# Optimization experiments

Hardware: AMD Instinct MI355X
Metric: run time of the kernel (lower is better)

Reference implementation:

```python
import jax, jax.numpy as jnp
import numpy as np

B, L, H, NH, NB = 16, 200, 128, 2, 2
ITEMS, SPAN = 50000, 256
NEG = -2.0**32 + 1.0  # mask value used by the torch module


def _ln(x, g, b, eps=1e-8):
    m = jnp.mean(x, axis=-1, keepdims=True)
    v = jnp.mean((x - m) ** 2, axis=-1, keepdims=True)
    return (x - m) / jnp.sqrt(v + eps) * g + b


def setup_inputs() -> dict:
    key = jax.random.key(0)
    ks = jax.random.split(key, 20)
    p = lambda k, s: (jax.random.normal(k, s, jnp.float32) * 0.02)
    item_emb = p(ks[0], (ITEMS + 1, H)).at[0].set(0.0)  # padding_idx=0
    return {
        "user_ids": jax.random.randint(ks[1], (B,), 0, 10000),
        "log_seqs": jax.random.randint(ks[2], (B, L), 0, ITEMS),
        "time_matrices": jax.random.randint(ks[3], (B, L, L), 0, SPAN),
        "pos_seqs": jax.random.randint(ks[4], (B, L), 0, ITEMS),
        "neg_seqs": jax.random.randint(ks[5], (B, L), 0, ITEMS),
        "item_emb": item_emb,
        "pos_K_emb": p(ks[6], (L, H)),
        "pos_V_emb": p(ks[7], (L, H)),
        "time_K_emb": p(ks[8], (SPAN + 1, H)),
        "time_V_emb": p(ks[9], (SPAN + 1, H)),
        "Wq": p(ks[10], (NB, H, H)), "bq": jnp.zeros((NB, H)),
        "Wk": p(ks[11], (NB, H, H)), "bk": jnp.zeros((NB, H)),
        "Wv": p(ks[12], (NB, H, H)), "bv": jnp.zeros((NB, H)),
        "ln1_g": jnp.ones((NB, H)), "ln1_b": jnp.zeros((NB, H)),
        "W1": p(ks[13], (NB, H, H)), "b1": jnp.zeros((NB, H)),
        "W2": p(ks[14], (NB, H, H)), "b2": jnp.zeros((NB, H)),
        "ln2_g": jnp.ones((NB, H)), "ln2_b": jnp.zeros((NB, H)),
        "lnf_g": jnp.ones((H,)), "lnf_b": jnp.zeros((H,)),
    }


def reference(user_ids, log_seqs, time_matrices, pos_seqs, neg_seqs,
              item_emb, pos_K_emb, pos_V_emb, time_K_emb, time_V_emb,
              Wq, bq, Wk, bk, Wv, bv, ln1_g, ln1_b,
              W1, b1, W2, b2, ln2_g, ln2_b, lnf_g, lnf_b):
    d = H // NH
    pad = (log_seqs == 0)                    # (B,L) timeline mask
    keep = (~pad)[..., None].astype(jnp.float32)

    seqs = item_emb[log_seqs] * jnp.sqrt(jnp.float32(H))
    seqs = seqs * keep
    posK = pos_K_emb.reshape(L, NH, d)       # same for every batch element
    posV = pos_V_emb.reshape(L, NH, d)
    tmK = time_K_emb[time_matrices].reshape(B, L, L, NH, d)  # (B,L,L,h,d)
    tmV = time_V_emb[time_matrices].reshape(B, L, L, NH, d)
    causal = ~jnp.tril(jnp.ones((L, L), dtype=bool))          # True = masked
    mask = pad[:, None, :, None] | causal[None, None, :, :]   # (B,1,L,L) row-mask | causal

    for i in range(NB):
        Q = (seqs @ Wq[i].T + bq[i]).reshape(B, L, NH, d)
        K = (seqs @ Wk[i].T + bk[i]).reshape(B, L, NH, d)
        V = (seqs @ Wv[i].T + bv[i]).reshape(B, L, NH, d)
        aw = jnp.einsum('bqhd,bkhd->bhqk', Q, K)
        aw = aw + jnp.einsum('bqhd,khd->bhqk', Q, posK)
        aw = aw + jnp.einsum('bqkhd,bqhd->bhqk', tmK, Q)
        aw = aw / jnp.sqrt(jnp.float32(d))
        aw = jnp.where(mask, NEG, aw)
        A = jax.nn.softmax(aw, axis=-1)                        # (B,h,L,L)
        out = jnp.einsum('bhqk,bkhd->bqhd', A, V)
        out = out + jnp.einsum('bhqk,khd->bqhd', A, posV)
        out = out + jnp.einsum('bhqk,bqkhd->bqhd', A, tmV)
        out = out.reshape(B, L, H)
        seqs = _ln(seqs + out, ln1_g[i], ln1_b[i])
        ffn = jax.nn.relu(seqs @ W1[i].T + b1[i]) @ W2[i].T + b2[i]
        seqs = _ln(seqs + ffn, ln2_g[i], ln2_b[i])
        seqs = seqs * keep

    log_feats = _ln(seqs, lnf_g, lnf_b)
    pos_logits = jnp.sum(log_feats * item_emb[pos_seqs], axis=-1)  # (B,L)
    neg_logits = jnp.sum(log_feats * item_emb[neg_seqs], axis=-1)
    return jnp.stack([pos_logits, neg_logits])  # (2,B,L)
```

## Files before the change

### kernel.cpp

```cpp
#include <hip/hip_runtime.h>
#include <hip/hip_bf16.h>
#include <math.h>

#define BB 16
#define LL 200
#define HH 128
#define DD 64
#define QT2 8
#define NQT2 25
#define NEGF -4294967295.0f
#define SQRTH 11.313708498984761f

__global__ __launch_bounds__(512) void k_qkv(float* __restrict__ seqs,
    const int* __restrict__ log_seqs, const float* __restrict__ item_emb, int do_embed,
    const float* __restrict__ Wq, const float* __restrict__ bq,
    const float* __restrict__ Wk, const float* __restrict__ bk,
    const float* __restrict__ Wv, const float* __restrict__ bv,
    const float* __restrict__ posK, const float* __restrict__ posV,
    float* __restrict__ Q, float* __restrict__ Kp, float* __restrict__ Vp) {
    __shared__ float s_lds[16][HH];
    int r0g = blockIdx.x * 16;
    int t = threadIdx.x;
    if (do_embed) {
        int r = t >> 5, d4 = t & 31;
        int id = log_seqs[r0g + r];
        float4 v = make_float4(0.f, 0.f, 0.f, 0.f);
        if (id != 0) {
            v = ((const float4*)(item_emb + id * HH))[d4];
            v.x *= SQRTH; v.y *= SQRTH; v.z *= SQRTH; v.w *= SQRTH;
        }
        *(float4*)&s_lds[r][d4 * 4] = v;
        ((float4*)(seqs + r0g * HH))[t] = v;
    } else {
        ((float4*)s_lds)[t] = ((const float4*)(seqs + r0g * HH))[t];
    }
    __syncthreads();
    int c = t & 127, rg = t >> 7;
    float aq[4] = {0.f, 0.f, 0.f, 0.f};
    float ak[4] = {0.f, 0.f, 0.f, 0.f};
    float av[4] = {0.f, 0.f, 0.f, 0.f};
    const float4* wq4 = (const float4*)(Wq + c * HH);
    const float4* wk4 = (const float4*)(Wk + c * HH);
    const float4* wv4 = (const float4*)(Wv + c * HH);
#pragma unroll 4
    for (int k4 = 0; k4 < HH / 4; ++k4) {
        float4 wq = wq4[k4], wk = wk4[k4], wv = wv4[k4];
#pragma unroll
        for (int r = 0; r < 4; ++r) {
            float4 s = *(const float4*)&s_lds[rg * 4 + r][k4 * 4];
            aq[r] += s.x * wq.x + s.y * wq.y + s.z * wq.z + s.w * wq.w;
            ak[r] += s.x * wk.x + s.y * wk.y + s.z * wk.z + s.w * wk.w;
            av[r] += s.x * wv.x + s.y * wv.y + s.z * wv.z + s.w * wv.w;
        }
    }
#pragma unroll
    for (int r = 0; r < 4; ++r) {
        int row = r0g + rg * 4 + r;
        int l = row % LL;
        Q[row * HH + c]  = aq[r] + bq[c];
        Kp[row * HH + c] = ak[r] + bk[c] + posK[l * HH + c];
        Vp[row * HH + c] = av[r] + bv[c] + posV[l * HH + c];
    }
}

__global__ __launch_bounds__(256) void k_proj(const float* __restrict__ Q,
    const float* __restrict__ timeK, float* __restrict__ projK) {
    int bh = blockIdx.x / 13, qt = blockIdx.x % 13;
    int b = bh >> 1, h = bh & 1;
    int qlo = qt * 16;
    __shared__ float Qs[16][68];
    __shared__ float TK[32][68];
    int t = threadIdx.x;
    {
        int r = t >> 4, d4 = t & 15;
        int q = qlo + r;
        float4 v = make_float4(0.f, 0.f, 0.f, 0.f);
        if (q < LL) v = ((const float4*)(Q + (b * LL + q) * HH + h * DD))[d4];
        *(float4*)&Qs[r][d4 * 4] = v;
    }
    int tq = t >> 4, ttl = t & 15;
    int q = qlo + tq;
    for (int c = 0; c < 9; ++c) {
        int base = c * 32;
        __syncthreads();
        for (int x = t; x < 512; x += 256) {
            int i = x >> 4, d4 = x & 15;
            int tt = base + i;
            if (tt < 257)
                *(float4*)&TK[i][d4 * 4] =
                    ((const float4*)(timeK + tt * HH + h * DD))[d4];
        }
        __syncthreads();
#pragma unroll
        for (int j = 0; j < 2; ++j) {
            int ti = ttl + 16 * j;
            int tt = base + ti;
            if (tt < 257 && q < LL) {
                float acc = 0.f;
#pragma unroll
                for (int d4 = 0; d4 < 16; ++d4) {
                    float4 qv = *(const float4*)&Qs[tq][d4 * 4];
                    float4 kv = *(const float4*)&TK[ti][d4 * 4];
                    acc += qv.x * kv.x + qv.y * kv.y + qv.z * kv.z + qv.w * kv.w;
                }
                projK[(bh * LL + q) * 257 + tt] = acc;
            }
        }
    }
}

__global__ __launch_bounds__(256) void k_attn(
    const float* __restrict__ Q, const float* __restrict__ Kp, const float* __restrict__ Vp,
    const float* __restrict__ projK, const float* __restrict__ timeV,
    const int* __restrict__ tm, const int* __restrict__ log_seqs,
    float* __restrict__ attnout) {
    int bh = blockIdx.x / NQT2, qt = blockIdx.x % NQT2;
    int b = bh >> 1, h = bh & 1;
    int qlo = qt * QT2;
    __shared__ float K_s[32][68];
    __shared__ float smemW[457 * 12];
    __shared__ unsigned long long pm64[4];
    __shared__ int s_allmask;
#define WT(i, j) smemW[(i) * 12 + (j)]
    int t = threadIdx.x;
    int tq = t >> 5, lane = t & 31, g = tq;
    int q = qlo + tq;
    int qhi = qlo + QT2 - 1;

    {
        bool keep = (t < LL) && (log_seqs[b * LL + t] != 0);
        unsigned long long ball = __ballot(keep);
        if ((t & 63) == 0) pm64[t >> 6] = ball;
    }
    if (t == 0) s_allmask = 0;
    for (int x = t; x < 200 * 12; x += 256) smemW[x] = NEGF;
    for (int x = 200 * 12 + t; x < 457 * 12; x += 256) smemW[x] = 0.f;
    float4 qreg[16];
    {
        const float4* qp = (const float4*)(Q + (b * LL + q) * HH + h * DD);
#pragma unroll
        for (int d4 = 0; d4 < 16; ++d4) qreg[d4] = qp[d4];
    }
    const int* tmrow = tm + (b * LL + q) * LL;
    const float* projrow = projK + (bh * LL + q) * 257;
    __syncthreads();

    int nkc = (qhi >> 5) + 1;
    for (int kc = 0; kc < nkc; ++kc) {
        int kbase = kc * 32;
        for (int x = t; x < 512; x += 256) {
            int i = x >> 4, d4 = x & 15;
            int k = kbase + i;
            if (k < LL)
                *(float4*)&K_s[i][d4 * 4] =
                    ((const float4*)(Kp + (b * LL + k) * HH + h * DD))[d4];
        }
        __syncthreads();
        int k = kbase + lane;
        if (k <= q && ((pm64[k >> 6] >> (k & 63)) & 1ull)) {
            float acc = 0.f;
#pragma unroll
            for (int d4 = 0; d4 < 16; ++d4) {
                float4 kv = *(const float4*)&K_s[lane][d4 * 4];
                acc += qreg[d4].x * kv.x + qreg[d4].y * kv.y +
                       qreg[d4].z * kv.z + qreg[d4].w * kv.w;
            }
            WT(k, tq) = (acc + projrow[tmrow[k]]) * 0.125f;
        }
        __syncthreads();
    }

    float mx = -INFINITY;
    for (int k = lane; k < LL; k += 32) mx = fmaxf(mx, WT(k, tq));
    mx = fmaxf(mx, __shfl_xor(mx, 1, 64));
    mx = fmaxf(mx, __shfl_xor(mx, 2, 64));
    mx = fmaxf(mx, __shfl_xor(mx, 4, 64));
    mx = fmaxf(mx, __shfl_xor(mx, 8, 64));
    mx = fmaxf(mx, __shfl_xor(mx, 16, 64));
    bool allmask = (mx == NEGF);
    float sum = 0.f;
    for (int k = lane; k < LL; k += 32) {
        float e = __expf(WT(k, tq) - mx);
        WT(k, tq) = e;
        sum += e;
    }
    sum += __shfl_xor(sum, 1, 64);
    sum += __shfl_xor(sum, 2, 64);
    sum += __shfl_xor(sum, 4, 64);
    sum += __shfl_xor(sum, 8, 64);
    sum += __shfl_xor(sum, 16, 64);
    float inv = 1.0f / sum;
    int klim = allmask ? LL : (q + 1);
    if (allmask && lane == 0) s_allmask = 1;
    for (int k = lane; k < LL; k += 32) {
        float p = WT(k, tq) * inv;
        WT(k, tq) = p;
        if (k < klim) atomicAdd(&WT(200 + tmrow[k], tq), p);
    }
    __syncthreads();

    int kmax = s_allmask ? LL : (qhi + 1);
    float a00=0.f,a01=0.f,a10=0.f,a11=0.f,a20=0.f,a21=0.f,a30=0.f,a31=0.f;
    float a40=0.f,a41=0.f,a50=0.f,a51=0.f,a60=0.f,a61=0.f,a70=0.f,a71=0.f;
#define PV_STEP(WROW, SRCPTR)                                            \
    {                                                                    \
        const float* wr = &WROW;                                         \
        float4 w0 = *(const float4*)wr;                                  \
        float4 w1 = *(const float4*)(wr + 4);                            \
        float2 vv = *(const float2*)(SRCPTR);                            \
        a00 += w0.x * vv.x; a01 += w0.x * vv.y;                          \
        a10 += w0.y * vv.x; a11 += w0.y * vv.y;                          \
        a20 += w0.z * vv.x; a21 += w0.z * vv.y;                          \
        a30 += w0.w * vv.x; a31 += w0.w * vv.y;                          \
        a40 += w1.x * vv.x; a41 += w1.x * vv.y;                          \
        a50 += w1.y * vv.x; a51 += w1.y * vv.y;                          \
        a60 += w1.z * vv.x; a61 += w1.z * vv.y;                          \
        a70 += w1.w * vv.x; a71 += w1.w * vv.y;                          \
    }
    for (int i = g; i < kmax; i += 8)
        PV_STEP(WT(i, 0), Vp + (b * LL + i) * HH + h * DD + lane * 2);
    for (int i = g; i < 257; i += 8)
        PV_STEP(WT(200 + i, 0), timeV + i * HH + h * DD + lane * 2);
#undef PV_STEP
    __syncthreads();
    float* part = smemW;
    part[g * 512 + 0 * 64 + lane * 2] = a00; part[g * 512 + 0 * 64 + lane * 2 + 1] = a01;
    part[g * 512 + 1 * 64 + lane * 2] = a10; part[g * 512 + 1 * 64 + lane * 2 + 1] = a11;
    part[g * 512 + 2 * 64 + lane * 2] = a20; part[g * 512 + 2 * 64 + lane * 2 + 1] = a21;
    part[g * 512 + 3 * 64 + lane * 2] = a30; part[g * 512 + 3 * 64 + lane * 2 + 1] = a31;
    part[g * 512 + 4 * 64 + lane * 2] = a40; part[g * 512 + 4 * 64 + lane * 2 + 1] = a41;
    part[g * 512 + 5 * 64 + lane * 2] = a50; part[g * 512 + 5 * 64 + lane * 2 + 1] = a51;
    part[g * 512 + 6 * 64 + lane * 2] = a60; part[g * 512 + 6 * 64 + lane * 2 + 1] = a61;
    part[g * 512 + 7 * 64 + lane * 2] = a70; part[g * 512 + 7 * 64 + lane * 2 + 1] = a71;
    __syncthreads();
    {
        float ox = 0.f, oy = 0.f;
#pragma unroll
        for (int gg = 0; gg < 8; ++gg) {
            ox += part[gg * 512 + tq * 64 + lane * 2];
            oy += part[gg * 512 + tq * 64 + lane * 2 + 1];
        }
        *(float2*)(attnout + (b * LL + q) * HH + h * DD + lane * 2) =
            make_float2(ox, oy);
    }
#undef WT
}

__global__ __launch_bounds__(512) void k_ffn_full(
    float* __restrict__ seqs, const float* __restrict__ AO,
    const float* __restrict__ g1, const float* __restrict__ be1,
    const float* __restrict__ W1, const float* __restrict__ b1,
    const float* __restrict__ W2, const float* __restrict__ b2,
    const float* __restrict__ g2, const float* __restrict__ be2,
    const int* __restrict__ log_seqs, int do_final,
    const float* __restrict__ lnf_g, const float* __restrict__ lnf_b,
    const float* __restrict__ item_emb,
    const int* __restrict__ pos_seqs, const int* __restrict__ neg_seqs,
    float* __restrict__ out) {
    __shared__ float s_lds[16][HH];
    __shared__ float h_lds[16][HH];
    int r0g = blockIdx.x * 16;
    int t = threadIdx.x;
    {
        float4 a = ((const float4*)(seqs + r0g * HH))[t];
        float4 o = ((const float4*)(AO + r0g * HH))[t];
        a.x += o.x; a.y += o.y; a.z += o.z; a.w += o.w;
        ((float4*)s_lds)[t] = a;
    }
    __syncthreads();
    int w = t >> 6, lane = t & 63;
    int lrow = w * 2 + (lane >> 5), cl = lane & 31;
    {
        float sm = 0.f;
#pragma unroll
        for (int j = 0; j < 4; ++j) sm += s_lds[lrow][cl + 32 * j];
        sm += __shfl_xor(sm, 1, 64);
        sm += __shfl_xor(sm, 2, 64);
        sm += __shfl_xor(sm, 4, 64);
        sm += __shfl_xor(sm, 8, 64);
        sm += __shfl_xor(sm, 16, 64);
        float mean = sm * (1.0f / HH);
        float vr = 0.f;
#pragma unroll
        for (int j = 0; j < 4; ++j) {
            float d = s_lds[lrow][cl + 32 * j] - mean;
            vr += d * d;
        }
        vr += __shfl_xor(vr, 1, 64);
        vr += __shfl_xor(vr, 2, 64);
        vr += __shfl_xor(vr, 4, 64);
        vr += __shfl_xor(vr, 8, 64);
        vr += __shfl_xor(vr, 16, 64);
        float rstd = rsqrtf(vr * (1.0f / HH) + 1e-8f);
#pragma unroll
        for (int j = 0; j < 4; ++j) {
            int c = cl + 32 * j;
            s_lds[lrow][c] = (s_lds[lrow][c] - mean) * rstd * g1[c] + be1[c];
        }
    }
    __syncthreads();
    int c = t & 127, rg = t >> 7;
    float acc[4] = {0.f, 0.f, 0.f, 0.f};
    const float4* w14 = (const float4*)(W1 + c * HH);
#pragma unroll 4
    for (int k4 = 0; k4 < HH / 4; ++k4) {
        float4 ww = w14[k4];
#pragma unroll
        for (int r = 0; r < 4; ++r) {
            float4 s = *(const float4*)&s_lds[rg * 4 + r][k4 * 4];
            acc[r] += s.x * ww.x + s.y * ww.y + s.z * ww.z + s.w * ww.w;
        }
    }
#pragma unroll
    for (int r = 0; r < 4; ++r) h_lds[rg * 4 + r][c] = fmaxf(acc[r] + b1[c], 0.f);
    __syncthreads();
#pragma unroll
    for (int r = 0; r < 4; ++r) acc[r] = 0.f;
    const float4* w24 = (const float4*)(W2 + c * HH);
#pragma unroll 4
    for (int k4 = 0; k4 < HH / 4; ++k4) {
        float4 ww = w24[k4];
#pragma unroll
        for (int r = 0; r < 4; ++r) {
            float4 s = *(const float4*)&h_lds[rg * 4 + r][k4 * 4];
            acc[r] += s.x * ww.x + s.y * ww.y + s.z * ww.z + s.w * ww.w;
        }
    }
    __syncthreads();
#pragma unroll
    for (int r = 0; r < 4; ++r)
        h_lds[rg * 4 + r][c] = s_lds[rg * 4 + r][c] + acc[r] + b2[c];
    __syncthreads();
    {
        float sm = 0.f;
#pragma unroll
        for (int j = 0; j < 4; ++j) sm += h_lds[lrow][cl + 32 * j];
        sm += __shfl_xor(sm, 1, 64);
        sm += __shfl_xor(sm, 2, 64);
        sm += __shfl_xor(sm, 4, 64);
        sm += __shfl_xor(sm, 8, 64);
        sm += __shfl_xor(sm, 16, 64);
        float mean = sm * (1.0f / HH);
        float vr = 0.f;
#pragma unroll
        for (int j = 0; j < 4; ++j) {
            float d = h_lds[lrow][cl + 32 * j] - mean;
            vr += d * d;
        }
        vr += __shfl_xor(vr, 1, 64);
        vr += __shfl_xor(vr, 2, 64);
        vr += __shfl_xor(vr, 4, 64);
        vr += __shfl_xor(vr, 8, 64);
        vr += __shfl_xor(vr, 16, 64);
        float rstd = rsqrtf(vr * (1.0f / HH) + 1e-8f);
        int row = r0g + lrow;
        float keep = (log_seqs[row] != 0) ? 1.0f : 0.0f;
        float y2[4];
#pragma unroll
        for (int j = 0; j < 4; ++j) {
            int cc = cl + 32 * j;
            y2[j] = ((h_lds[lrow][cc] - mean) * rstd * g2[cc] + be2[cc]) * keep;
        }
        if (!do_final) {
#pragma unroll
            for (int j = 0; j < 4; ++j)
                seqs[row * HH + cl + 32 * j] = y2[j];
        } else {
            float sm2 = y2[0] + y2[1] + y2[2] + y2[3];
            sm2 += __shfl_xor(sm2, 1, 64);
            sm2 += __shfl_xor(sm2, 2, 64);
            sm2 += __shfl_xor(sm2, 4, 64);
            sm2 += __shfl_xor(sm2, 8, 64);
            sm2 += __shfl_xor(sm2, 16, 64);
            float mean2 = sm2 * (1.0f / HH);
            float vr2 = 0.f;
#pragma unroll
            for (int j = 0; j < 4; ++j) {
                float d = y2[j] - mean2;
                vr2 += d * d;
            }
            vr2 += __shfl_xor(vr2, 1, 64);
            vr2 += __shfl_xor(vr2, 2, 64);
            vr2 += __shfl_xor(vr2, 4, 64);
            vr2 += __shfl_xor(vr2, 8, 64);
            vr2 += __shfl_xor(vr2, 16, 64);
            float rstd2 = rsqrtf(vr2 * (1.0f / HH) + 1e-8f);
            int pid = pos_seqs[row];
            int nid = neg_seqs[row];
            float pp = 0.f, nn = 0.f;
#pragma unroll
            for (int j = 0; j < 4; ++j) {
                int cc = cl + 32 * j;
                float lf = (y2[j] - mean2) * rstd2 * lnf_g[cc] + lnf_b[cc];
                pp += lf * item_emb[pid * HH + cc];
                nn += lf * item_emb[nid * HH + cc];
            }
            pp += __shfl_xor(pp, 1, 64);
            pp += __shfl_xor(pp, 2, 64);
            pp += __shfl_xor(pp, 4, 64);
            pp += __shfl_xor(pp, 8, 64);
            pp += __shfl_xor(pp, 16, 64);
            nn += __shfl_xor(nn, 1, 64);
            nn += __shfl_xor(nn, 2, 64);
            nn += __shfl_xor(nn, 4, 64);
            nn += __shfl_xor(nn, 8, 64);
            nn += __shfl_xor(nn, 16, 64);
            if (cl == 0) {
                out[row] = pp;
                out[BB * LL + row] = nn;
            }
        }
    }
}

extern "C" void kernel_launch(void* const* d_in, const int* in_sizes, int n_in,
                              void* d_out, int out_size, void* d_ws, size_t ws_size,
                              hipStream_t stream) {
    const int* log_seqs = (const int*)d_in[1];
    const int* tm       = (const int*)d_in[2];
    const int* pos_seqs = (const int*)d_in[3];
    const int* neg_seqs = (const int*)d_in[4];
    const float* item_emb = (const float*)d_in[5];
    const float* posK   = (const float*)d_in[6];
    const float* posV   = (const float*)d_in[7];
    const float* timeK  = (const float*)d_in[8];
    const float* timeV  = (const float*)d_in[9];
    const float* Wq = (const float*)d_in[10];
    const float* bq = (const float*)d_in[11];
    const float* Wk = (const float*)d_in[12];
    const float* bk = (const float*)d_in[13];
    const float* Wv = (const float*)d_in[14];
    const float* bv = (const float*)d_in[15];
    const float* ln1_g = (const float*)d_in[16];
    const float* ln1_b = (const float*)d_in[17];
    const float* W1 = (const float*)d_in[18];
    const float* b1 = (const float*)d_in[19];
    const float* W2 = (const float*)d_in[20];
    const float* b2 = (const float*)d_in[21];
    const float* ln2_g = (const float*)d_in[22];
    const float* ln2_b = (const float*)d_in[23];
    const float* lnf_g = (const float*)d_in[24];
    const float* lnf_b = (const float*)d_in[25];

    float* ws    = (float*)d_ws;
    float* seqs  = ws;
    float* Qb    = seqs + 409600;
    float* Kpb   = Qb + 409600;
    float* Vpb   = Kpb + 409600;
    float* AO    = Vpb + 409600;
    float* projK = AO + 409600;

    for (int i = 0; i < 2; ++i) {
        k_qkv<<<BB * LL / 16, 512, 0, stream>>>(seqs, log_seqs, item_emb,
            (i == 0) ? 1 : 0,
            Wq + i * HH * HH, bq + i * HH,
            Wk + i * HH * HH, bk + i * HH,
            Wv + i * HH * HH, bv + i * HH,
            posK, posV, Qb, Kpb, Vpb);
        k_proj<<<32 * 13, 256, 0, stream>>>(Qb, timeK, projK);
        k_attn<<<32 * NQT2, 256, 0, stream>>>(Qb, Kpb, Vpb, projK, timeV,
                                              tm, log_seqs, AO);
        k_ffn_full<<<BB * LL / 16, 512, 0, stream>>>(seqs, AO,
            ln1_g + i * HH, ln1_b + i * HH,
            W1 + i * HH * HH, b1 + i * HH,
            W2 + i * HH * HH, b2 + i * HH,
            ln2_g + i * HH, ln2_b + i * HH, log_seqs,
            (i == 1) ? 1 : 0, lnf_g, lnf_b, item_emb,
            pos_seqs, neg_seqs, (float*)d_out);
    }
}
```

Baseline: 197.8 us.

## Shrink per-block row tiles across all kernels to raise grid parallelism

All four kernels now take smaller row or query tiles. QKV and FFN blocks handle 4 rows instead of 16, the projection handles 8 queries instead of 16, and attention handles 4 queries with 128 threads instead of 8 with 256. QKV now gives each of three 128-thread groups one of the Q, K or V weight matrices. Attention reads the padding mask from global memory instead of building a ballot bitmask, and reuses the K tile buffer for the partial-sum reduction. The goal is many more blocks to fill the GPU's compute units, at the cost of reading each weight matrix from memory more times per block and less reuse of shared tiles.

```diff
diff --git a/kernel.cpp b/kernel.cpp
--- a/kernel.cpp
+++ b/kernel.cpp
@@ -6,82 +6,83 @@
 #define LL 200
 #define HH 128
 #define DD 64
-#define QT2 8
-#define NQT2 25
+#define NQT4 50
 #define NEGF -4294967295.0f
 #define SQRTH 11.313708498984761f
 
-__global__ __launch_bounds__(512) void k_qkv(float* __restrict__ seqs,
+__global__ __launch_bounds__(384) void k_qkv(float* __restrict__ seqs,
     const int* __restrict__ log_seqs, const float* __restrict__ item_emb, int do_embed,
     const float* __restrict__ Wq, const float* __restrict__ bq,
     const float* __restrict__ Wk, const float* __restrict__ bk,
     const float* __restrict__ Wv, const float* __restrict__ bv,
     const float* __restrict__ posK, const float* __restrict__ posV,
     float* __restrict__ Q, float* __restrict__ Kp, float* __restrict__ Vp) {
-    __shared__ float s_lds[16][HH];
-    int r0g = blockIdx.x * 16;
+    __shared__ float s_lds[4][HH];
+    int r0g = blockIdx.x * 4;
     int t = threadIdx.x;
-    if (do_embed) {
+    if (t < 128) {
         int r = t >> 5, d4 = t & 31;
-        int id = log_seqs[r0g + r];
-        float4 v = make_float4(0.f, 0.f, 0.f, 0.f);
-        if (id != 0) {
-            v = ((const float4*)(item_emb + id * HH))[d4];
-            v.x *= SQRTH; v.y *= SQRTH; v.z *= SQRTH; v.w *= SQRTH;
-        }
-        *(float4*)&s_lds[r][d4 * 4] = v;
-        ((float4*)(seqs + r0g * HH))[t] = v;
-    } else {
-        ((float4*)s_lds)[t] = ((const float4*)(seqs + r0g * HH))[t];
-    }
-    __syncthreads();
-    int c = t & 127, rg = t >> 7;
-    float aq[4] = {0.f, 0.f, 0.f, 0.f};
-    float ak[4] = {0.f, 0.f, 0.f, 0.f};
-    float av[4] = {0.f, 0.f, 0.f, 0.f};
-    const float4* wq4 = (const float4*)(Wq + c * HH);
-    const float4* wk4 = (const float4*)(Wk + c * HH);
-    const float4* wv4 = (const float4*)(Wv + c * HH);
-#pragma unroll 4
-    for (int k4 = 0; k4 < HH / 4; ++k4) {
-        float4 wq = wq4[k4], wk = wk4[k4], wv = wv4[k4];
-#pragma unroll
-        for (int r = 0; r < 4; ++r) {
-            float4 s = *(const float4*)&s_lds[rg * 4 + r][k4 * 4];
-            aq[r] += s.x * wq.x + s.y * wq.y + s.z * wq.z + s.w * wq.w;
-            ak[r] += s.x * wk.x + s.y * wk.y + s.z * wk.z + s.w * wk.w;
-            av[r] += s.x * wv.x + s.y * wv.y + s.z * wv.z + s.w * wv.w;
-        }
-    }
+        if (do_embed) {
+            int id = log_seqs[r0g + r];
+            float4 v = make_float4(0.f, 0.f, 0.f, 0.f);
+            if (id != 0) {
+                v = ((const float4*)(item_emb + id * HH))[d4];
+                v.x *= SQRTH; v.y *= SQRTH; v.z *= SQRTH; v.w *= SQRTH;
+            }
+            *(float4*)&s_lds[r][d4 * 4] = v;
+            ((float4*)(seqs + r0g * HH))[t] = v;
+        } else {
+            ((float4*)s_lds)[t] = ((const float4*)(seqs + r0g * HH))[t];
+        }
+    }
+    __syncthreads();
+    int which = t >> 7, col = t & 127;
+    const float* W = (which == 0) ? Wq : (which == 1) ? Wk : Wv;
+    float a0 = 0.f, a1 = 0.f, a2 = 0.f, a3 = 0.f;
+    const float4* w4 = (const float4*)(W + col * HH);
+#pragma unroll 8
+    for (int k4 = 0; k4 < 32; ++k4) {
+        float4 w = w4[k4];
+        float4 s0 = *(const float4*)&s_lds[0][k4 * 4];
+        float4 s1 = *(const float4*)&s_lds[1][k4 * 4];
+        float4 s2 = *(const float4*)&s_lds[2][k4 * 4];
+        float4 s3 = *(const float4*)&s_lds[3][k4 * 4];
+        a0 += s0.x * w.x + s0.y * w.y + s0.z * w.z + s0.w * w.w;
+        a1 += s1.x * w.x + s1.y * w.y + s1.z * w.z + s1.w * w.w;
+        a2 += s2.x * w.x + s2.y * w.y + s2.z * w.z + s2.w * w.w;
+        a3 += s3.x * w.x + s3.y * w.y + s3.z * w.z + s3.w * w.w;
+    }
+    float a[4] = {a0, a1, a2, a3};
 #pragma unroll
     for (int r = 0; r < 4; ++r) {
-        int row = r0g + rg * 4 + r;
+        int row = r0g + r;
         int l = row % LL;
-        Q[row * HH + c]  = aq[r] + bq[c];
-        Kp[row * HH + c] = ak[r] + bk[c] + posK[l * HH + c];
-        Vp[row * HH + c] = av[r] + bv[c] + posV[l * HH + c];
+        if (which == 0) {
+            Q[row * HH + col] = a[r] + bq[col];
+        } else if (which == 1) {
+            Kp[row * HH + col] = a[r] + bk[col] + posK[l * HH + col];
+        } else {
+            Vp[row * HH + col] = a[r] + bv[col] + posV[l * HH + col];
+        }
     }
 }
 
 __global__ __launch_bounds__(256) void k_proj(const float* __restrict__ Q,
     const float* __restrict__ timeK, float* __restrict__ projK) {
-    int bh = blockIdx.x / 13, qt = blockIdx.x % 13;
+    int bh = blockIdx.x / 25, qt = blockIdx.x % 25;
     int b = bh >> 1, h = bh & 1;
-    int qlo = qt * 16;
-    __shared__ float Qs[16][68];
+    int qlo = qt * 8;
+    __shared__ float Qs[8][68];
     __shared__ float TK[32][68];
     int t = threadIdx.x;
-    {
+    if (t < 128) {
         int r = t >> 4, d4 = t & 15;
-        int q = qlo + r;
-        float4 v = make_float4(0.f, 0.f, 0.f, 0.f);
-        if (q < LL) v = ((const float4*)(Q + (b * LL + q) * HH + h * DD))[d4];
-        *(float4*)&Qs[r][d4 * 4] = v;
-    }
-    int tq = t >> 4, ttl = t & 15;
-    int q = qlo + tq;
-    for (int c = 0; c < 9; ++c) {
-        int base = c * 32;
+        *(float4*)&Qs[r][d4 * 4] =
+            ((const float4*)(Q + (b * LL + qlo + r) * HH + h * DD))[d4];
+    }
+    int tq = t >> 5, ttl = t & 31;
+    for (int ch = 0; ch < 9; ++ch) {
+        int base = ch * 32;
         __syncthreads();
         for (int x = t; x < 512; x += 256) {
             int i = x >> 4, d4 = x & 15;
@@ -91,50 +92,40 @@
                     ((const float4*)(timeK + tt * HH + h * DD))[d4];
         }
         __syncthreads();
+        int tt = base + ttl;
+        if (tt < 257) {
+            float acc = 0.f;
 #pragma unroll
-        for (int j = 0; j < 2; ++j) {
-            int ti = ttl + 16 * j;
-            int tt = base + ti;
-            if (tt < 257 && q < LL) {
-                float acc = 0.f;
-#pragma unroll
-                for (int d4 = 0; d4 < 16; ++d4) {
-                    float4 qv = *(const float4*)&Qs[tq][d4 * 4];
-                    float4 kv = *(const float4*)&TK[ti][d4 * 4];
-                    acc += qv.x * kv.x + qv.y * kv.y + qv.z * kv.z + qv.w * kv.w;
-                }
-                projK[(bh * LL + q) * 257 + tt] = acc;
+            for (int d4 = 0; d4 < 16; ++d4) {
+                float4 qv = *(const float4*)&Qs[tq][d4 * 4];
+                float4 kv = *(const float4*)&TK[ttl][d4 * 4];
+                acc += qv.x * kv.x + qv.y * kv.y + qv.z * kv.z + qv.w * kv.w;
             }
+            projK[(bh * LL + qlo + tq) * 257 + tt] = acc;
         }
     }
 }
 
-__global__ __launch_bounds__(256) void k_attn(
+__global__ __launch_bounds__(128) void k_attn(
     const float* __restrict__ Q, const float* __restrict__ Kp, const float* __restrict__ Vp,
     const float* __restrict__ projK, const float* __restrict__ timeV,
     const int* __restrict__ tm, const int* __restrict__ log_seqs,
     float* __restrict__ attnout) {
-    int bh = blockIdx.x / NQT2, qt = blockIdx.x % NQT2;
+    int bh = blockIdx.x / NQT4, qt = blockIdx.x % NQT4;
     int b = bh >> 1, h = bh & 1;
-    int qlo = qt * QT2;
+    int qlo = qt * 4;
     __shared__ float K_s[32][68];
-    __shared__ float smemW[457 * 12];
-    __shared__ unsigned long long pm64[4];
+    __shared__ float smemW[457 * 8];
     __shared__ int s_allmask;
-#define WT(i, j) smemW[(i) * 12 + (j)]
+#define WT(i, j) smemW[(i) * 8 + (j)]
     int t = threadIdx.x;
     int tq = t >> 5, lane = t & 31, g = tq;
     int q = qlo + tq;
-    int qhi = qlo + QT2 - 1;
-
-    {
-        bool keep = (t < LL) && (log_seqs[b * LL + t] != 0);
-        unsigned long long ball = __ballot(keep);
-        if ((t & 63) == 0) pm64[t >> 6] = ball;
-    }
+    int qhi = qlo + 3;
+
     if (t == 0) s_allmask = 0;
-    for (int x = t; x < 200 * 12; x += 256) smemW[x] = NEGF;
-    for (int x = 200 * 12 + t; x < 457 * 12; x += 256) smemW[x] = 0.f;
+    for (int x = t; x < 200 * 8; x += 128) smemW[x] = NEGF;
+    for (int x = 200 * 8 + t; x < 457 * 8; x += 128) smemW[x] = 0.f;
     float4 qreg[16];
     {
         const float4* qp = (const float4*)(Q + (b * LL + q) * HH + h * DD);
@@ -143,12 +134,13 @@
     }
     const int* tmrow = tm + (b * LL + q) * LL;
     const float* projrow = projK + (bh * LL + q) * 257;
+    const int* lsrow = log_seqs + b * LL;
     __syncthreads();
 
     int nkc = (qhi >> 5) + 1;
     for (int kc = 0; kc < nkc; ++kc) {
         int kbase = kc * 32;
-        for (int x = t; x < 512; x += 256) {
+        for (int x = t; x < 512; x += 128) {
             int i = x >> 4, d4 = x & 15;
             int k = kbase + i;
             if (k < LL)
@@ -157,7 +149,7 @@
         }
         __syncthreads();
         int k = kbase + lane;
-        if (k <= q && ((pm64[k >> 6] >> (k & 63)) & 1ull)) {
+        if (k <= q && lsrow[k] != 0) {
             float acc = 0.f;
 #pragma unroll
             for (int d4 = 0; d4 < 16; ++d4) {
@@ -200,45 +192,34 @@
     __syncthreads();
 
     int kmax = s_allmask ? LL : (qhi + 1);
-    float a00=0.f,a01=0.f,a10=0.f,a11=0.f,a20=0.f,a21=0.f,a30=0.f,a31=0.f;
-    float a40=0.f,a41=0.f,a50=0.f,a51=0.f,a60=0.f,a61=0.f,a70=0.f,a71=0.f;
-#define PV_STEP(WROW, SRCPTR)                                            \
+    float a0x=0.f,a0y=0.f,a1x=0.f,a1y=0.f,a2x=0.f,a2y=0.f,a3x=0.f,a3y=0.f;
+#define PV_STEP(WIDX, SRCPTR)                                            \
     {                                                                    \
-        const float* wr = &WROW;                                         \
-        float4 w0 = *(const float4*)wr;                                  \
-        float4 w1 = *(const float4*)(wr + 4);                            \
+        float4 w = *(const float4*)&smemW[(WIDX) * 8];                   \
         float2 vv = *(const float2*)(SRCPTR);                            \
-        a00 += w0.x * vv.x; a01 += w0.x * vv.y;                          \
-        a10 += w0.y * vv.x; a11 += w0.y * vv.y;                          \
-        a20 += w0.z * vv.x; a21 += w0.z * vv.y;                          \
-        a30 += w0.w * vv.x; a31 += w0.w * vv.y;                          \
-        a40 += w1.x * vv.x; a41 += w1.x * vv.y;                          \
-        a50 += w1.y * vv.x; a51 += w1.y * vv.y;                          \
-        a60 += w1.z * vv.x; a61 += w1.z * vv.y;                          \
-        a70 += w1.w * vv.x; a71 += w1.w * vv.y;                          \
-    }
-    for (int i = g; i < kmax; i += 8)
-        PV_STEP(WT(i, 0), Vp + (b * LL + i) * HH + h * DD + lane * 2);
-    for (int i = g; i < 257; i += 8)
-        PV_STEP(WT(200 + i, 0), timeV + i * HH + h * DD + lane * 2);
+        a0x += w.x * vv.x; a0y += w.x * vv.y;                            \
+        a1x += w.y * vv.x; a1y += w.y * vv.y;                            \
+        a2x += w.z * vv.x; a2y += w.z * vv.y;                            \
+        a3x += w.w * vv.x; a3y += w.w * vv.y;                            \
+    }
+    for (int i = g; i < kmax; i += 4)
+        PV_STEP(i, Vp + (b * LL + i) * HH + h * DD + lane * 2);
+    for (int i = g; i < 257; i += 4)
+        PV_STEP(200 + i, timeV + i * HH + h * DD + lane * 2);
 #undef PV_STEP
     __syncthreads();
-    float* part = smemW;
-    part[g * 512 + 0 * 64 + lane * 2] = a00; part[g * 512 + 0 * 64 + lane * 2 + 1] = a01;
-    part[g * 512 + 1 * 64 + lane * 2] = a10; part[g * 512 + 1 * 64 + lane * 2 + 1] = a11;
-    part[g * 512 + 2 * 64 + lane * 2] = a20; part[g * 512 + 2 * 64 + lane * 2 + 1] = a21;
-    part[g * 512 + 3 * 64 + lane * 2] = a30; part[g * 512 + 3 * 64 + lane * 2 + 1] = a31;
-    part[g * 512 + 4 * 64 + lane * 2] = a40; part[g * 512 + 4 * 64 + lane * 2 + 1] = a41;
-    part[g * 512 + 5 * 64 + lane * 2] = a50; part[g * 512 + 5 * 64 + lane * 2 + 1] = a51;
-    part[g * 512 + 6 * 64 + lane * 2] = a60; part[g * 512 + 6 * 64 + lane * 2 + 1] = a61;
-    part[g * 512 + 7 * 64 + lane * 2] = a70; part[g * 512 + 7 * 64 + lane * 2 + 1] = a71;
+    float* part = &K_s[0][0];
+    part[g * 256 + 0 * 64 + lane * 2] = a0x; part[g * 256 + 0 * 64 + lane * 2 + 1] = a0y;
+    part[g * 256 + 1 * 64 + lane * 2] = a1x; part[g * 256 + 1 * 64 + lane * 2 + 1] = a1y;
+    part[g * 256 + 2 * 64 + lane * 2] = a2x; part[g * 256 + 2 * 64 + lane * 2 + 1] = a2y;
+    part[g * 256 + 3 * 64 + lane * 2] = a3x; part[g * 256 + 3 * 64 + lane * 2 + 1] = a3y;
     __syncthreads();
     {
         float ox = 0.f, oy = 0.f;
 #pragma unroll
-        for (int gg = 0; gg < 8; ++gg) {
-            ox += part[gg * 512 + tq * 64 + lane * 2];
-            oy += part[gg * 512 + tq * 64 + lane * 2 + 1];
+        for (int gg = 0; gg < 4; ++gg) {
+            ox += part[gg * 256 + tq * 64 + lane * 2];
+            oy += part[gg * 256 + tq * 64 + lane * 2 + 1];
         }
         *(float2*)(attnout + (b * LL + q) * HH + h * DD + lane * 2) =
             make_float2(ox, oy);
@@ -246,7 +227,7 @@
 #undef WT
 }
 
-__global__ __launch_bounds__(512) void k_ffn_full(
+__global__ __launch_bounds__(256) void k_ffn_full(
     float* __restrict__ seqs, const float* __restrict__ AO,
     const float* __restrict__ g1, const float* __restrict__ be1,
     const float* __restrict__ W1, const float* __restrict__ b1,
@@ -257,155 +238,108 @@
     const float* __restrict__ item_emb,
     const int* __restrict__ pos_seqs, const int* __restrict__ neg_seqs,
     float* __restrict__ out) {
-    __shared__ float s_lds[16][HH];
-    __shared__ float h_lds[16][HH];
-    int r0g = blockIdx.x * 16;
+    __shared__ float s_lds[4][HH];
+    __shared__ float h_lds[4][HH];
+    int r0g = blockIdx.x * 4;
     int t = threadIdx.x;
-    {
+    if (t < 128) {
         float4 a = ((const float4*)(seqs + r0g * HH))[t];
         float4 o = ((const float4*)(AO + r0g * HH))[t];
         a.x += o.x; a.y += o.y; a.z += o.z; a.w += o.w;
         ((float4*)s_lds)[t] = a;
     }
     __syncthreads();
-    int w = t >> 6, lane = t & 63;
-    int lrow = w * 2 + (lane >> 5), cl = lane & 31;
+    int wv = t >> 6, lane = t & 63;
     {
-        float sm = 0.f;
-#pragma unroll
-        for (int j = 0; j < 4; ++j) sm += s_lds[lrow][cl + 32 * j];
-        sm += __shfl_xor(sm, 1, 64);
-        sm += __shfl_xor(sm, 2, 64);
-        sm += __shfl_xor(sm, 4, 64);
-        sm += __shfl_xor(sm, 8, 64);
-        sm += __shfl_xor(sm, 16, 64);
+        float x0 = s_lds[wv][lane], x1 = s_lds[wv][lane + 64];
+        float sm = x0 + x1;
+        sm += __shfl_xor(sm, 1, 64);  sm += __shfl_xor(sm, 2, 64);
+        sm += __shfl_xor(sm, 4, 64);  sm += __shfl_xor(sm, 8, 64);
+        sm += __shfl_xor(sm, 16, 64); sm += __shfl_xor(sm, 32, 64);
         float mean = sm * (1.0f / HH);
-        float vr = 0.f;
-#pragma unroll
-        for (int j = 0; j < 4; ++j) {
-            float d = s_lds[lrow][cl + 32 * j] - mean;
-            vr += d * d;
-        }
-        vr += __shfl_xor(vr, 1, 64);
-        vr += __shfl_xor(vr, 2, 64);
-        vr += __shfl_xor(vr, 4, 64);
-        vr += __shfl_xor(vr, 8, 64);
-        vr += __shfl_xor(vr, 16, 64);
+        float d0 = x0 - mean, d1 = x1 - mean;
+        float vr = d0 * d0 + d1 * d1;
+        vr += __shfl_xor(vr, 1, 64);  vr += __shfl_xor(vr, 2, 64);
+        vr += __shfl_xor(vr, 4, 64);  vr += __shfl_xor(vr, 8, 64);
+        vr += __shfl_xor(vr, 16, 64); vr += __shfl_xor(vr, 32, 64);
         float rstd = rsqrtf(vr * (1.0f / HH) + 1e-8f);
-#pragma unroll
-        for (int j = 0; j < 4; ++j) {
-            int c = cl + 32 * j;
-            s_lds[lrow][c] = (s_lds[lrow][c] - mean) * rstd * g1[c] + be1[c];
-        }
-    }
-    __syncthreads();
-    int c = t & 127, rg = t >> 7;
-    float acc[4] = {0.f, 0.f, 0.f, 0.f};
-    const float4* w14 = (const float4*)(W1 + c * HH);
-#pragma unroll 4
-    for (int k4 = 0; k4 < HH / 4; ++k4) {
-        float4 ww = w14[k4];
-#pragma unroll
-        for (int r = 0; r < 4; ++r) {
-            float4 s = *(const float4*)&s_lds[rg * 4 + r][k4 * 4];
-            acc[r] += s.x * ww.x + s.y * ww.y + s.z * ww.z + s.w * ww.w;
-        }
-    }
-#pragma unroll
-    for (int r = 0; r < 4; ++r) h_lds[rg * 4 + r][c] = fmaxf(acc[r] + b1[c], 0.f);
-    __syncthreads();
-#pragma unroll
-    for (int r = 0; r < 4; ++r) acc[r] = 0.f;
-    const float4* w24 = (const float4*)(W2 + c * HH);
-#pragma unroll 4
-    for (int k4 = 0; k4 < HH / 4; ++k4) {
-        float4 ww = w24[k4];
-#pragma unroll
-        for (int r = 0; r < 4; ++r) {
-            float4 s = *(const float4*)&h_lds[rg * 4 + r][k4 * 4];
-            acc[r] += s.x * ww.x + s.y * ww.y + s.z * ww.z + s.w * ww.w;
-        }
-    }
-    __syncthreads();
-#pragma unroll
-    for (int r = 0; r < 4; ++r)
-        h_lds[rg * 4 + r][c] = s_lds[rg * 4 + r][c] + acc[r] + b2[c];
+        s_lds[wv][lane]      = d0 * rstd * g1[lane] + be1[lane];
+        s_lds[wv][lane + 64] = d1 * rstd * g1[lane + 64] + be1[lane + 64];
+    }
+    __syncthreads();
+    int col = t & 127, rg = t >> 7;
+    float ac0 = 0.f, ac1 = 0.f;
+    const float4* w14 = (const float4*)(W1 + col * HH);
+#pragma unroll 8
+    for (int k4 = 0; k4 < 32; ++k4) {
+        float4 w = w14[k4];
+        float4 s0 = *(const float4*)&s_lds[rg * 2][k4 * 4];
+        float4 s1 = *(const float4*)&s_lds[rg * 2 + 1][k4 * 4];
+        ac0 += s0.x * w.x + s0.y * w.y + s0.z * w.z + s0.w * w.w;
+        ac1 += s1.x * w.x + s1.y * w.y + s1.z * w.z + s1.w * w.w;
+    }
+    h_lds[rg * 2][col]     = fmaxf(ac0 + b1[col], 0.f);
+    h_lds[rg * 2 + 1][col] = fmaxf(ac1 + b1[col], 0.f);
+    __syncthreads();
+    ac0 = 0.f; ac1 = 0.f;
+    const float4* w24 = (const float4*)(W2 + col * HH);
+#pragma unroll 8
+    for (int k4 = 0; k4 < 32; ++k4) {
+        float4 w = w24[k4];
+        float4 s0 = *(const float4*)&h_lds[rg * 2][k4 * 4];
+        float4 s1 = *(const float4*)&h_lds[rg * 2 + 1][k4 * 4];
+        ac0 += s0.x * w.x + s0.y * w.y + s0.z * w.z + s0.w * w.w;
+        ac1 += s1.x * w.x + s1.y * w.y + s1.z * w.z + s1.w * w.w;
+    }
+    __syncthreads();
+    h_lds[rg * 2][col]     = s_lds[rg * 2][col] + ac0 + b2[col];
+    h_lds[rg * 2 + 1][col] = s_lds[rg * 2 + 1][col] + ac1 + b2[col];
     __syncthreads();
     {
-        float sm = 0.f;
-#pragma unroll
-        for (int j = 0; j < 4; ++j) sm += h_lds[lrow][cl + 32 * j];
-        sm += __shfl_xor(sm, 1, 64);
-        sm += __shfl_xor(sm, 2, 64);
-        sm += __shfl_xor(sm, 4, 64);
-        sm += __shfl_xor(sm, 8, 64);
-        sm += __shfl_xor(sm, 16, 64);
+        float x0 = h_lds[wv][lane], x1 = h_lds[wv][lane + 64];
+        float sm = x0 + x1;
+        sm += __shfl_xor(sm, 1, 64);  sm += __shfl_xor(sm, 2, 64);
+        sm += __shfl_xor(sm, 4, 64);  sm += __shfl_xor(sm, 8, 64);
+        sm += __shfl_xor(sm, 16, 64); sm += __shfl_xor(sm, 32, 64);
         float mean = sm * (1.0f / HH);
-        float vr = 0.f;
-#pragma unroll
-        for (int j = 0; j < 4; ++j) {
-            float d = h_lds[lrow][cl + 32 * j] - mean;
-            vr += d * d;
-        }
-        vr += __shfl_xor(vr, 1, 64);
-        vr += __shfl_xor(vr, 2, 64);
-        vr += __shfl_xor(vr, 4, 64);
-        vr += __shfl_xor(vr, 8, 64);
-        vr += __shfl_xor(vr, 16, 64);
+        float d0 = x0 - mean, d1 = x1 - mean;
+        float vr = d0 * d0 + d1 * d1;
+        vr += __shfl_xor(vr, 1, 64);  vr += __shfl_xor(vr, 2, 64);
+        vr += __shfl_xor(vr, 4, 64);  vr += __shfl_xor(vr, 8, 64);
+        vr += __shfl_xor(vr, 16, 64); vr += __shfl_xor(vr, 32, 64);
         float rstd = rsqrtf(vr * (1.0f / HH) + 1e-8f);
-        int row = r0g + lrow;
+        int row = r0g + wv;
         float keep = (log_seqs[row] != 0) ? 1.0f : 0.0f;
-        float y2[4];
-#pragma unroll
-        for (int j = 0; j < 4; ++j) {
-            int cc = cl + 32 * j;
-            y2[j] = ((h_lds[lrow][cc] - mean) * rstd * g2[cc] + be2[cc]) * keep;
-        }
+        float y0 = (d0 * rstd * g2[lane] + be2[lane]) * keep;
+        float y1 = (d1 * rstd * g2[lane + 64] + be2[lane + 64]) * keep;
         if (!do_final) {
-#pragma unroll
-            for (int j = 0; j < 4; ++j)
-                seqs[row * HH + cl + 32 * j] = y2[j];
+            seqs[row * HH + lane]      = y0;
+            seqs[row * HH + lane + 64] = y1;
         } else {
-            float sm2 = y2[0] + y2[1] + y2[2] + y2[3];
-            sm2 += __shfl_xor(sm2, 1, 64);
-            sm2 += __shfl_xor(sm2, 2, 64);
-            sm2 += __shfl_xor(sm2, 4, 64);
-            sm2 += __shfl_xor(sm2, 8, 64);
-            sm2 += __shfl_xor(sm2, 16, 64);
+            float sm2 = y0 + y1;
+            sm2 += __shfl_xor(sm2, 1, 64);  sm2 += __shfl_xor(sm2, 2, 64);
+            sm2 += __shfl_xor(sm2, 4, 64);  sm2 += __shfl_xor(sm2, 8, 64);
+            sm2 += __shfl_xor(sm2, 16, 64); sm2 += __shfl_xor(sm2, 32, 64);
             float mean2 = sm2 * (1.0f / HH);
-            float vr2 = 0.f;
-#pragma unroll
-            for (int j = 0; j < 4; ++j) {
-                float d = y2[j] - mean2;
-                vr2 += d * d;
-            }
-            vr2 += __shfl_xor(vr2, 1, 64);
-            vr2 += __shfl_xor(vr2, 2, 64);
-            vr2 += __shfl_xor(vr2, 4, 64);
-            vr2 += __shfl_xor(vr2, 8, 64);
-            vr2 += __shfl_xor(vr2, 16, 64);
+            float e0 = y0 - mean2, e1 = y1 - mean2;
+            float vr2 = e0 * e0 + e1 * e1;
+            vr2 += __shfl_xor(vr2, 1, 64);  vr2 += __shfl_xor(vr2, 2, 64);
+            vr2 += __shfl_xor(vr2, 4, 64);  vr2 += __shfl_xor(vr2, 8, 64);
+            vr2 += __shfl_xor(vr2, 16, 64); vr2 += __shfl_xor(vr2, 32, 64);
             float rstd2 = rsqrtf(vr2 * (1.0f / HH) + 1e-8f);
             int pid = pos_seqs[row];
             int nid = neg_seqs[row];
-            float pp = 0.f, nn = 0.f;
-#pragma unroll
-            for (int j = 0; j < 4; ++j) {
-                int cc = cl + 32 * j;
-                float lf = (y2[j] - mean2) * rstd2 * lnf_g[cc] + lnf_b[cc];
-                pp += lf * item_emb[pid * HH + cc];
-                nn += lf * item_emb[nid * HH + cc];
-            }
-            pp += __shfl_xor(pp, 1, 64);
-            pp += __shfl_xor(pp, 2, 64);
-            pp += __shfl_xor(pp, 4, 64);
-            pp += __shfl_xor(pp, 8, 64);
-            pp += __shfl_xor(pp, 16, 64);
-            nn += __shfl_xor(nn, 1, 64);
-            nn += __shfl_xor(nn, 2, 64);
-            nn += __shfl_xor(nn, 4, 64);
-            nn += __shfl_xor(nn, 8, 64);
-            nn += __shfl_xor(nn, 16, 64);
-            if (cl == 0) {
+            float lf0 = e0 * rstd2 * lnf_g[lane] + lnf_b[lane];
+            float lf1 = e1 * rstd2 * lnf_g[lane + 64] + lnf_b[lane + 64];
+            float pp = lf0 * item_emb[pid * HH + lane] + lf1 * item_emb[pid * HH + lane + 64];
+            float nn = lf0 * item_emb[nid * HH + lane] + lf1 * item_emb[nid * HH + lane + 64];
+            pp += __shfl_xor(pp, 1, 64);  pp += __shfl_xor(pp, 2, 64);
+            pp += __shfl_xor(pp, 4, 64);  pp += __shfl_xor(pp, 8, 64);
+            pp += __shfl_xor(pp, 16, 64); pp += __shfl_xor(pp, 32, 64);
+            nn += __shfl_xor(nn, 1, 64);  nn += __shfl_xor(nn, 2, 64);
+            nn += __shfl_xor(nn, 4, 64);  nn += __shfl_xor(nn, 8, 64);
+            nn += __shfl_xor(nn, 16, 64); nn += __shfl_xor(nn, 32, 64);
+            if (lane == 0) {
                 out[row] = pp;
                 out[BB * LL + row] = nn;
             }
@@ -451,16 +385,16 @@
     float* projK = AO + 409600;
 
     for (int i = 0; i < 2; ++i) {
-        k_qkv<<<BB * LL / 16, 512, 0, stream>>>(seqs, log_seqs, item_emb,
+        k_qkv<<<BB * LL / 4, 384, 0, stream>>>(seqs, log_seqs, item_emb,
             (i == 0) ? 1 : 0,
             Wq + i * HH * HH, bq + i * HH,
             Wk + i * HH * HH, bk + i * HH,
             Wv + i * HH * HH, bv + i * HH,
             posK, posV, Qb, Kpb, Vpb);
-        k_proj<<<32 * 13, 256, 0, stream>>>(Qb, timeK, projK);
-        k_attn<<<32 * NQT2, 256, 0, stream>>>(Qb, Kpb, Vpb, projK, timeV,
+        k_proj<<<32 * 25, 256, 0, stream>>>(Qb, timeK, projK);
+        k_attn<<<32 * NQT4, 128, 0, stream>>>(Qb, Kpb, Vpb, projK, timeV,
                                               tm, log_seqs, AO);
-        k_ffn_full<<<BB * LL / 16, 512, 0, stream>>>(seqs, AO,
+        k_ffn_full<<<BB * LL / 4, 256, 0, stream>>>(seqs, AO,
             ln1_g + i * HH, ln1_b + i * HH,
             W1 + i * HH * HH, b1 + i * HH,
             W2 + i * HH * HH, b2 + i * HH,
```

After: 271.5 us. +37.3%, slower.
